# Kernel tuning notes

Measured on AMD Instinct MI355X. Metric: run time of the kernel, lower is better.

The kernel has to match this reference:

```python
import jax, jax.numpy as jnp
from jax import lax
import numpy as np


def setup_inputs() -> dict:
    key = jax.random.key(0)
    ks = jax.random.split(key, 9)
    B, T_enc, D = 32, 2048, 512   # batch, encoder length, enc_dim == nb_dims
    T_dec, U = 128, 512           # decode steps, LSTM units (== out_dim)
    s = 0.05
    return {
        "enc_output": jax.random.normal(ks[0], (B, T_enc, D), jnp.float32),
        "dec_input": jax.random.normal(ks[1], (B, T_dec, U), jnp.float32),
        "W1": jax.random.normal(ks[2], (D, D), jnp.float32) * s,
        "W2": jax.random.normal(ks[3], (U, D), jnp.float32) * s,
        "b2": jnp.zeros((D,), jnp.float32),
        "V": jax.random.normal(ks[4], (D,), jnp.float32) * s,
        "W3": jax.random.normal(ks[5], (D + U, U), jnp.float32) * s,
        "b3": jnp.zeros((U,), jnp.float32),
        "lstm_kernel": jax.random.normal(ks[6], (U, 4 * U), jnp.float32) * s,
        "lstm_rec_kernel": jax.random.normal(ks[7], (U, 4 * U), jnp.float32) * s,
        "lstm_bias": jnp.zeros((4 * U,), jnp.float32),
    }


def reference(enc_output, dec_input, W1, W2, b2, V, W3, b3,
              lstm_kernel, lstm_rec_kernel, lstm_bias):
    # Precomputed constant, as in get_constants(): xW1 = enc_output @ W1
    xW1 = jnp.einsum('bte,ed->btd', enc_output, W1)  # [B, T_enc, D]

    def step(carry, x_t):
        h, c = carry                                  # [B, U] each
        # Bahdanau additive attention score over encoder positions
        hW2 = h @ W2 + b2                             # [B, D]
        u = jnp.tanh(xW1 + hW2[:, None, :])           # [B, T_enc, D]
        scores = jnp.einsum('btd,d->bt', u, V)        # [B, T_enc]
        a = jax.nn.softmax(scores, axis=1)            # [B, T_enc]
        Xa = jnp.einsum('bt,bte->be', a, enc_output)  # [B, D]
        # Mix decoder input with context, then LSTM cell step
        h_in = jnp.concatenate([x_t, Xa], axis=1) @ W3 + b3  # [B, U]
        z = h_in @ lstm_kernel + h @ lstm_rec_kernel + lstm_bias
        zi, zf, zg, zo = jnp.split(z, 4, axis=1)
        i = jax.nn.sigmoid(zi)
        f = jax.nn.sigmoid(zf)
        g = jnp.tanh(zg)
        o = jax.nn.sigmoid(zo)
        c_new = f * c + i * g
        h_new = o * jnp.tanh(c_new)
        return (h_new, c_new), h_new

    B = enc_output.shape[0]
    U = W3.shape[1]
    h0 = jnp.zeros((B, U), enc_output.dtype)
    c0 = jnp.zeros((B, U), enc_output.dtype)
    xs = jnp.swapaxes(dec_input, 0, 1)                # [T_dec, B, U]
    _, ys = lax.scan(step, (h0, c0), xs)              # ys: [T_dec, B, U]
    return jnp.swapaxes(ys, 0, 1)                     # [B, T_dec, U]
```

## Files before the change

kernel.cpp:

```cpp
#include <hip/hip_runtime.h>
#include <hip/hip_cooperative_groups.h>
#include <cstddef>
#include <cstdint>

namespace cg = cooperative_groups;

#define B 32
#define TENC 2048
#define TDEC 128
#define NCH 8
#define TCH 256

typedef unsigned short ushort_t;
typedef __attribute__((ext_vector_type(8))) short short8;
typedef __attribute__((ext_vector_type(4))) float floatx4;

__device__ __forceinline__ uint16_t f2bf(float x) {
    uint32_t u = __float_as_uint(x);
    u += 0x7fffu + ((u >> 16) & 1u);
    return (uint16_t)(u >> 16);
}
__device__ __forceinline__ float bf2f(ushort_t u) {
    return __uint_as_float(((uint32_t)u) << 16);
}
__device__ __forceinline__ void unpack8(uint4 v, float* f) {
    f[0] = __uint_as_float(v.x << 16); f[1] = __uint_as_float(v.x & 0xffff0000u);
    f[2] = __uint_as_float(v.y << 16); f[3] = __uint_as_float(v.y & 0xffff0000u);
    f[4] = __uint_as_float(v.z << 16); f[5] = __uint_as_float(v.z & 0xffff0000u);
    f[6] = __uint_as_float(v.w << 16); f[7] = __uint_as_float(v.w & 0xffff0000u);
}
__device__ __forceinline__ float fast_tanh(float x) {
    float e = __expf(2.f * x);
    return 1.f - 2.f * __builtin_amdgcn_rcpf(e + 1.f);
}
__device__ __forceinline__ float fast_sig(float x) {
    return __builtin_amdgcn_rcpf(1.f + __expf(-x));
}

__global__ void cvt_kernel(const float* __restrict__ in, ushort_t* __restrict__ out) {
    int i = blockIdx.x * 256 + threadIdx.x;
    const float4* ip = (const float4*)in;
    float4 a = ip[2 * i], b = ip[2 * i + 1];
    uint4 o;
    o.x = (uint32_t)f2bf(a.x) | ((uint32_t)f2bf(a.y) << 16);
    o.y = (uint32_t)f2bf(a.z) | ((uint32_t)f2bf(a.w) << 16);
    o.z = (uint32_t)f2bf(b.x) | ((uint32_t)f2bf(b.y) << 16);
    o.w = (uint32_t)f2bf(b.z) | ((uint32_t)f2bf(b.w) << 16);
    ((uint4*)out)[i] = o;
}

__global__ void tr_cvt_bf16_kernel(const float* __restrict__ in, ushort_t* __restrict__ out,
                                   int R, int C) {
    __shared__ float tile[32][33];
    int r0 = blockIdx.y * 32, c0 = blockIdx.x * 32;
    int tx = threadIdx.x & 31, ty = threadIdx.x >> 5;
#pragma unroll
    for (int i = 0; i < 4; i++) {
        int r = ty + i * 8;
        tile[r][tx] = in[(size_t)(r0 + r) * C + c0 + tx];
    }
    __syncthreads();
#pragma unroll
    for (int i = 0; i < 4; i++) {
        int rr = ty + i * 8;
        out[(size_t)(c0 + rr) * R + r0 + tx] = f2bf(tile[tx][rr]);
    }
}
__global__ void tr_f32_kernel(const float* __restrict__ in, float* __restrict__ out,
                              int R, int C) {
    __shared__ float tile[32][33];
    int r0 = blockIdx.y * 32, c0 = blockIdx.x * 32;
    int tx = threadIdx.x & 31, ty = threadIdx.x >> 5;
#pragma unroll
    for (int i = 0; i < 4; i++) {
        int r = ty + i * 8;
        tile[r][tx] = in[(size_t)(r0 + r) * C + c0 + tx];
    }
    __syncthreads();
#pragma unroll
    for (int i = 0; i < 4; i++) {
        int rr = ty + i * 8;
        out[(size_t)(c0 + rr) * R + r0 + tx] = tile[tx][rr];
    }
}

__global__ void bz_kernel(const float* __restrict__ b3, const float* __restrict__ Wk,
                          const float* __restrict__ bias, float* __restrict__ bz) {
    int g = blockIdx.x * 256 + threadIdx.x;
    float s = bias[g];
#pragma unroll 8
    for (int u = 0; u < 512; u++) s += b3[u] * Wk[(size_t)u * 2048 + g];
    bz[g] = s;
}

template <int BF16OUT>
__global__ void mfma_gemm_kernel(const ushort_t* __restrict__ A, const ushort_t* __restrict__ Bt,
                                 void* __restrict__ C, int M, int N) {
    int tid = threadIdx.x, wave = tid >> 6, lane = tid & 63;
    int wy = wave & 1, wx = wave >> 1;
    int m0 = blockIdx.y * 64 + wy * 32;
    int n0 = blockIdx.x * 64 + wx * 32;
    int lr = lane & 15, quad = lane >> 4;
    floatx4 a00 = {0.f, 0.f, 0.f, 0.f}, a01 = a00, a10 = a00, a11 = a00;
    const short8* Ap0 = (const short8*)(A + (size_t)(m0 + lr) * 512 + quad * 8);
    const short8* Ap1 = (const short8*)(A + (size_t)(m0 + 16 + lr) * 512 + quad * 8);
    const short8* Bp0 = (const short8*)(Bt + (size_t)(n0 + lr) * 512 + quad * 8);
    const short8* Bp1 = (const short8*)(Bt + (size_t)(n0 + 16 + lr) * 512 + quad * 8);
#pragma unroll 4
    for (int k = 0; k < 16; k++) {
        short8 av0 = Ap0[k * 4], av1 = Ap1[k * 4];
        short8 bv0 = Bp0[k * 4], bv1 = Bp1[k * 4];
        a00 = __builtin_amdgcn_mfma_f32_16x16x32_bf16(av0, bv0, a00, 0, 0, 0);
        a01 = __builtin_amdgcn_mfma_f32_16x16x32_bf16(av0, bv1, a01, 0, 0, 0);
        a10 = __builtin_amdgcn_mfma_f32_16x16x32_bf16(av1, bv0, a10, 0, 0, 0);
        a11 = __builtin_amdgcn_mfma_f32_16x16x32_bf16(av1, bv1, a11, 0, 0, 0);
    }
    int rb = quad * 4;
    if (BF16OUT) {
        ushort_t* Cp = (ushort_t*)C;
#pragma unroll
        for (int r = 0; r < 4; r++) {
            Cp[(size_t)(m0 + rb + r) * N + n0 + lr] = f2bf(a00[r]);
            Cp[(size_t)(m0 + rb + r) * N + n0 + 16 + lr] = f2bf(a01[r]);
            Cp[(size_t)(m0 + 16 + rb + r) * N + n0 + lr] = f2bf(a10[r]);
            Cp[(size_t)(m0 + 16 + rb + r) * N + n0 + 16 + lr] = f2bf(a11[r]);
        }
    } else {
        float* Cp = (float*)C;
#pragma unroll
        for (int r = 0; r < 4; r++) {
            Cp[(size_t)(m0 + rb + r) * N + n0 + lr] = a00[r];
            Cp[(size_t)(m0 + rb + r) * N + n0 + 16 + lr] = a01[r];
            Cp[(size_t)(m0 + 16 + rb + r) * N + n0 + lr] = a10[r];
            Cp[(size_t)(m0 + 16 + rb + r) * N + n0 + 16 + lr] = a11[r];
        }
    }
}

__global__ __launch_bounds__(256, 1) void step_kernel(
    const ushort_t* __restrict__ xW1h, const ushort_t* __restrict__ ench,
    const ushort_t* __restrict__ Zxh, const float* __restrict__ bz,
    const float* __restrict__ W2t, const float* __restrict__ Wrt,
    const float* __restrict__ Wazt, const float* __restrict__ Vv,
    const float* __restrict__ b2,
    float* __restrict__ h, float* __restrict__ c, float* __restrict__ hW2,
    float* __restrict__ zbuf, float* __restrict__ pm, float* __restrict__ pl,
    float* __restrict__ pacc, float* __restrict__ Xa, float* __restrict__ out) {
    cg::grid_group grid = cg::this_grid();
    int bk = blockIdx.x, tid = threadIdx.x;
    int wave = tid >> 6, lane = tid & 63;
    __shared__ float smem[21560];

    for (int t = 0; t < TDEC; ++t) {
        {
            for (int idx = tid; idx < 16384; idx += 256)
                smem[(idx >> 9) * 513 + (idx & 511)] = h[idx];
            int n0 = bk * 10;
            for (int idx = tid; idx < 5120; idx += 256) {
                int cc = idx >> 9, d = idx & 511;
                int n = n0 + cc;
                const float* src = (n < 512) ? (W2t + (size_t)n * 512)
                                             : (Wrt + (size_t)(n - 512) * 512);
                smem[16416 + cc * 513 + d] = src[d];
            }
            __syncthreads();
            int q = tid & 3;
#pragma unroll
            for (int r = 0; r < 5; ++r) {
                int o = r * 64 + (tid >> 2);
                int cc = o >> 5, b = o & 31;
                const float* hrow = smem + b * 513;
                const float* wrow = smem + 16416 + cc * 513;
                float acc = 0.f;
#pragma unroll 8
                for (int i = 0; i < 128; ++i) {
                    int d = q + 4 * i;
                    acc += hrow[d] * wrow[d];
                }
                acc += __shfl_xor(acc, 1, 64);
                acc += __shfl_xor(acc, 2, 64);
                if (q == 0) {
                    int n = n0 + cc;
                    if (n < 512) {
                        hW2[b * 512 + n] = acc + b2[n];
                    } else {
                        int g = n - 512;
                        float zx = bf2f(Zxh[((size_t)(b * 128 + t)) * 2048 + g]);
                        zbuf[b * 2048 + g] = acc + zx + bz[g];
                    }
                }
            }
        }
        grid.sync();
        {
            int b = bk >> 3, ch = bk & 7;
            float hs[8], vs[8];
            {
                const float4* hp = (const float4*)(hW2 + b * 512 + lane * 8);
                float4 h0 = hp[0], h1 = hp[1];
                hs[0] = h0.x; hs[1] = h0.y; hs[2] = h0.z; hs[3] = h0.w;
                hs[4] = h1.x; hs[5] = h1.y; hs[6] = h1.z; hs[7] = h1.w;
                const float4* vp = (const float4*)(Vv + lane * 8);
                float4 v0 = vp[0], v1 = vp[1];
                vs[0] = v0.x; vs[1] = v0.y; vs[2] = v0.z; vs[3] = v0.w;
                vs[4] = v1.x; vs[5] = v1.y; vs[6] = v1.z; vs[7] = v1.w;
            }
            int t0 = ch * TCH + wave * 64;
            const uint4* xr = (const uint4*)xW1h + ((size_t)b * TENC + t0) * 64 + lane;
            const uint4* er = (const uint4*)ench + ((size_t)b * TENC + t0) * 64 + lane;
            float m = -INFINITY, l = 0.f;
            float acc[8] = {0.f, 0.f, 0.f, 0.f, 0.f, 0.f, 0.f, 0.f};
#pragma unroll 2
            for (int tt = 0; tt < 64; ++tt) {
                uint4 xv = xr[(size_t)tt * 64];
                uint4 ev = er[(size_t)tt * 64];
                float xf[8], ef[8];
                unpack8(xv, xf);
                float s = 0.f;
#pragma unroll
                for (int j = 0; j < 8; j++) s += fast_tanh(xf[j] + hs[j]) * vs[j];
#pragma unroll
                for (int off = 32; off >= 1; off >>= 1) s += __shfl_xor(s, off, 64);
                float mn = fmaxf(m, s);
                float sc = __expf(m - mn);
                float p = __expf(s - mn);
                l = l * sc + p;
                unpack8(ev, ef);
#pragma unroll
                for (int j = 0; j < 8; j++) acc[j] = acc[j] * sc + p * ef[j];
                m = mn;
            }
            float* smv = smem;
            float* slv = smem + 8;
            float* sacc = smem + 16;
            if (lane == 0) { smv[wave] = m; slv[wave] = l; }
            __syncthreads();
            float bmx = fmaxf(fmaxf(smv[0], smv[1]), fmaxf(smv[2], smv[3]));
            float f = __expf(m - bmx);
#pragma unroll
            for (int j = 0; j < 8; j++) sacc[wave * 512 + lane * 8 + j] = acc[j] * f;
            __syncthreads();
            float s0 = sacc[tid] + sacc[512 + tid] + sacc[1024 + tid] + sacc[1536 + tid];
            float s1 = sacc[tid + 256] + sacc[512 + tid + 256] + sacc[1024 + tid + 256] +
                       sacc[1536 + tid + 256];
            size_t po = ((size_t)(b * NCH + ch)) * 512;
            pacc[po + tid] = s0;
            pacc[po + tid + 256] = s1;
            if (tid == 0) {
                pm[b * NCH + ch] = bmx;
                pl[b * NCH + ch] = slv[0] * __expf(smv[0] - bmx) + slv[1] * __expf(smv[1] - bmx) +
                                   slv[2] * __expf(smv[2] - bmx) + slv[3] * __expf(smv[3] - bmx);
            }
        }
        grid.sync();
        {
            int b = bk >> 3, ds0 = (bk & 7) * 64;
            if (tid < 64) {
                float mg = -1e30f;
#pragma unroll
                for (int i = 0; i < NCH; i++) mg = fmaxf(mg, pm[b * NCH + i]);
                float w[NCH];
                float L = 0.f;
#pragma unroll
                for (int i = 0; i < NCH; i++) {
                    w[i] = __expf(pm[b * NCH + i] - mg);
                    L += pl[b * NCH + i] * w[i];
                }
                float inv = __builtin_amdgcn_rcpf(L);
                int d = ds0 + tid;
                float s = 0.f;
#pragma unroll
                for (int i = 0; i < NCH; i++)
                    s += w[i] * pacc[((size_t)(b * NCH + i)) * 512 + d];
                Xa[b * 512 + d] = s * inv;
            }
        }
        grid.sync();
        {
            for (int idx = tid; idx < 16384; idx += 256)
                smem[(idx >> 9) * 513 + (idx & 511)] = Xa[idx];
            int u0 = bk * 2;
            for (int idx = tid; idx < 4096; idx += 256) {
                int rw = idx >> 9, d = idx & 511;
                int g = (rw >> 1) * 512 + u0 + (rw & 1);
                smem[16416 + rw * 513 + d] = Wazt[(size_t)g * 512 + d];
            }
            __syncthreads();
            int col = tid >> 5, b = tid & 31;
            const float* xrow = smem + b * 513;
            const float* wrow = smem + 16416 + col * 513;
            float acc = 0.f;
#pragma unroll 8
            for (int d = 0; d < 512; ++d) acc += xrow[d] * wrow[d];
            int g = (col >> 1) * 512 + u0 + (col & 1);
            smem[20800 + col * 32 + b] = acc + zbuf[b * 2048 + g];
            __syncthreads();
            if (tid < 64) {
                int bb = tid >> 1, uo = tid & 1;
                int u = u0 + uo;
                float zi = smem[20800 + (0 + uo) * 32 + bb];
                float zf = smem[20800 + (2 + uo) * 32 + bb];
                float zg = smem[20800 + (4 + uo) * 32 + bb];
                float zo = smem[20800 + (6 + uo) * 32 + bb];
                float ig = fast_sig(zi);
                float fg = fast_sig(zf);
                float gg = fast_tanh(zg);
                float og = fast_sig(zo);
                int idx = bb * 512 + u;
                float cn = fg * c[idx] + ig * gg;
                float hn = og * fast_tanh(cn);
                c[idx] = cn;
                h[idx] = hn;
                out[((size_t)bb * TDEC + t) * 512 + u] = hn;
            }
        }
        grid.sync();
    }
}

extern "C" void kernel_launch(void* const* d_in, const int* in_sizes, int n_in,
                              void* d_out, int out_size, void* d_ws, size_t ws_size,
                              hipStream_t stream) {
    const float* enc = (const float*)d_in[0];
    const float* dec = (const float*)d_in[1];
    const float* W1 = (const float*)d_in[2];
    const float* W2 = (const float*)d_in[3];
    const float* b2 = (const float*)d_in[4];
    const float* V = (const float*)d_in[5];
    const float* W3 = (const float*)d_in[6];
    const float* b3 = (const float*)d_in[7];
    const float* Wk = (const float*)d_in[8];
    const float* Wr = (const float*)d_in[9];
    const float* bias = (const float*)d_in[10];
    float* out = (float*)d_out;

    char* ws = (char*)d_ws;
    size_t o = 0;
    auto alloc = [&](size_t bytes) {
        void* p = ws + o;
        o += (bytes + 255) & ~(size_t)255;
        return p;
    };
    ushort_t* xW1h = (ushort_t*)alloc(67108864);
    ushort_t* ench = (ushort_t*)alloc(67108864);
    ushort_t* Zxh = (ushort_t*)alloc(16777216);
    ushort_t* dech = (ushort_t*)alloc(4194304);
    ushort_t* T1h = (ushort_t*)alloc(4194304);
    ushort_t* W1t = (ushort_t*)alloc(524288);
    ushort_t* W3h = (ushort_t*)alloc(1048576);
    ushort_t* W3at = (ushort_t*)alloc(524288);
    ushort_t* Wkt = (ushort_t*)alloc(2097152);
    float* W2t = (float*)alloc(1048576);
    float* Wrt = (float*)alloc(4194304);
    float* Wazt = (float*)alloc(4194304);
    float* bz = (float*)alloc(8192);
    float* h = (float*)alloc(65536);
    float* c = (float*)alloc(65536);
    float* hW2 = (float*)alloc(65536);
    float* Xa = (float*)alloc(65536);
    float* zbuf = (float*)alloc(262144);
    float* pm = (float*)alloc(1024);
    float* pl = (float*)alloc(1024);
    float* pacc = (float*)alloc(524288);

    hipMemsetAsync(h, 0, 131072, stream);

    cvt_kernel<<<16384, 256, 0, stream>>>(enc, ench);
    cvt_kernel<<<1024, 256, 0, stream>>>(dec, dech);
    cvt_kernel<<<256, 256, 0, stream>>>(W3, W3h);
    tr_cvt_bf16_kernel<<<dim3(16, 16), 256, 0, stream>>>(W1, W1t, 512, 512);
    tr_cvt_bf16_kernel<<<dim3(16, 16), 256, 0, stream>>>(W3, W3at, 512, 512);
    tr_cvt_bf16_kernel<<<dim3(64, 16), 256, 0, stream>>>(Wk, Wkt, 512, 2048);
    tr_f32_kernel<<<dim3(16, 16), 256, 0, stream>>>(W2, W2t, 512, 512);
    tr_f32_kernel<<<dim3(64, 16), 256, 0, stream>>>(Wr, Wrt, 512, 2048);
    bz_kernel<<<8, 256, 0, stream>>>(b3, Wk, bias, bz);
    mfma_gemm_kernel<1><<<dim3(8, 1024), 256, 0, stream>>>(ench, W1t, xW1h, 65536, 512);
    mfma_gemm_kernel<1><<<dim3(8, 64), 256, 0, stream>>>(dech, W3at, T1h, 4096, 512);
    mfma_gemm_kernel<1><<<dim3(32, 64), 256, 0, stream>>>(T1h, Wkt, Zxh, 4096, 2048);
    mfma_gemm_kernel<0><<<dim3(8, 32), 256, 0, stream>>>(Wkt, W3h + 512 * 512, Wazt, 2048, 512);

    void* args[] = {&xW1h, &ench, &Zxh, &bz, &W2t, &Wrt, &Wazt, &V, &b2,
                    &h, &c, &hW2, &zbuf, &pm, &pl, &pacc, &Xa, &out};
    hipLaunchCooperativeKernel((void*)step_kernel, dim3(256), dim3(256), args, 0, stream);
}
```

Measured before the change: 22.91 ms.

## Widen step kernel to 512 threads, drop softmax max, prefetch loads, use fp32 precompute

Doubles the cooperative step kernel to 512 threads (8 waves) and rebalances every phase for the extra waves. In the attention phase it drops the running-max rescaling of the online softmax and prefetches encoder rows with a four-deep register buffer, cutting exp and FMA work per position. It also computes the xW1 precompute with an fp32 SIMT GEMM instead of a bf16 MFMA GEMM, and keeps the Zx term in fp32. Together these aim at more latency hiding and less ALU work per step, likely for accuracy as well. The costs are a slower precompute GEMM and a softmax that relies on the scores staying small enough not to overflow exp.

After: 21.82 ms. 4.8% less time.

```diff
diff --git a/kernel.cpp b/kernel.cpp
--- a/kernel.cpp
+++ b/kernel.cpp
@@ -19,9 +19,6 @@
     uint32_t u = __float_as_uint(x);
     u += 0x7fffu + ((u >> 16) & 1u);
     return (uint16_t)(u >> 16);
-}
-__device__ __forceinline__ float bf2f(ushort_t u) {
-    return __uint_as_float(((uint32_t)u) << 16);
 }
 __device__ __forceinline__ void unpack8(uint4 v, float* f) {
     f[0] = __uint_as_float(v.x << 16); f[1] = __uint_as_float(v.x & 0xffff0000u);
@@ -91,6 +88,45 @@
 #pragma unroll 8
     for (int u = 0; u < 512; u++) s += b3[u] * Wk[(size_t)u * 2048 + g];
     bz[g] = s;
+}
+
+__global__ void gemm_xw1_kernel(const float* __restrict__ A, const float* __restrict__ Bm,
+                                ushort_t* __restrict__ C) {
+    __shared__ float As[16][68];
+    __shared__ float Bs[16][68];
+    int bm = blockIdx.y * 64, bn = blockIdx.x * 64;
+    int tx = threadIdx.x & 15, ty = threadIdx.x >> 4;
+    float acc[4][4] = {};
+    for (int k0 = 0; k0 < 512; k0 += 16) {
+#pragma unroll
+        for (int i = 0; i < 4; i++) {
+            int idx = threadIdx.x + 256 * i;
+            int r = idx >> 4, kk = idx & 15;
+            As[kk][r] = A[(size_t)(bm + r) * 512 + k0 + kk];
+            int cc = idx & 63, kb = idx >> 6;
+            Bs[kb][cc] = Bm[(size_t)(k0 + kb) * 512 + bn + cc];
+        }
+        __syncthreads();
+#pragma unroll
+        for (int kk = 0; kk < 16; kk++) {
+            float4 av = *(const float4*)&As[kk][ty * 4];
+            float4 bv = *(const float4*)&Bs[kk][tx * 4];
+            float a[4] = {av.x, av.y, av.z, av.w};
+            float b[4] = {bv.x, bv.y, bv.z, bv.w};
+#pragma unroll
+            for (int i = 0; i < 4; i++)
+#pragma unroll
+                for (int j = 0; j < 4; j++) acc[i][j] += a[i] * b[j];
+        }
+        __syncthreads();
+    }
+#pragma unroll
+    for (int i = 0; i < 4; i++) {
+        uint2 o;
+        o.x = (uint32_t)f2bf(acc[i][0]) | ((uint32_t)f2bf(acc[i][1]) << 16);
+        o.y = (uint32_t)f2bf(acc[i][2]) | ((uint32_t)f2bf(acc[i][3]) << 16);
+        *(uint2*)(C + (size_t)(bm + ty * 4 + i) * 512 + bn + tx * 4) = o;
+    }
 }
 
 template <int BF16OUT>
@@ -137,26 +173,34 @@
     }
 }
 
-__global__ __launch_bounds__(256, 1) void step_kernel(
+__global__ __launch_bounds__(512, 2) void step_kernel(
     const ushort_t* __restrict__ xW1h, const ushort_t* __restrict__ ench,
-    const ushort_t* __restrict__ Zxh, const float* __restrict__ bz,
+    const float* __restrict__ Zxf, const float* __restrict__ bz,
     const float* __restrict__ W2t, const float* __restrict__ Wrt,
     const float* __restrict__ Wazt, const float* __restrict__ Vv,
     const float* __restrict__ b2,
     float* __restrict__ h, float* __restrict__ c, float* __restrict__ hW2,
-    float* __restrict__ zbuf, float* __restrict__ pm, float* __restrict__ pl,
+    float* __restrict__ zbuf, float* __restrict__ pl,
     float* __restrict__ pacc, float* __restrict__ Xa, float* __restrict__ out) {
     cg::grid_group grid = cg::this_grid();
     int bk = blockIdx.x, tid = threadIdx.x;
     int wave = tid >> 6, lane = tid & 63;
     __shared__ float smem[21560];
 
+    float vs[8];
+    {
+        const float4* vp = (const float4*)(Vv + lane * 8);
+        float4 v0 = vp[0], v1 = vp[1];
+        vs[0] = v0.x; vs[1] = v0.y; vs[2] = v0.z; vs[3] = v0.w;
+        vs[4] = v1.x; vs[5] = v1.y; vs[6] = v1.z; vs[7] = v1.w;
+    }
+
     for (int t = 0; t < TDEC; ++t) {
         {
-            for (int idx = tid; idx < 16384; idx += 256)
+            for (int idx = tid; idx < 16384; idx += 512)
                 smem[(idx >> 9) * 513 + (idx & 511)] = h[idx];
             int n0 = bk * 10;
-            for (int idx = tid; idx < 5120; idx += 256) {
+            for (int idx = tid; idx < 5120; idx += 512) {
                 int cc = idx >> 9, d = idx & 511;
                 int n = n0 + cc;
                 const float* src = (n < 512) ? (W2t + (size_t)n * 512)
@@ -164,11 +208,13 @@
                 smem[16416 + cc * 513 + d] = src[d];
             }
             __syncthreads();
-            int q = tid & 3;
-#pragma unroll
-            for (int r = 0; r < 5; ++r) {
-                int o = r * 64 + (tid >> 2);
+            int q = tid & 3, slot = tid >> 2;
+#pragma unroll
+            for (int r = 0; r < 3; ++r) {
+                int o = r * 128 + slot;
+                bool valid = (o < 320);
                 int cc = o >> 5, b = o & 31;
+                if (cc > 9) cc = 9;
                 const float* hrow = smem + b * 513;
                 const float* wrow = smem + 16416 + cc * 513;
                 float acc = 0.f;
@@ -179,14 +225,14 @@
                 }
                 acc += __shfl_xor(acc, 1, 64);
                 acc += __shfl_xor(acc, 2, 64);
-                if (q == 0) {
+                if (q == 0 && valid) {
                     int n = n0 + cc;
                     if (n < 512) {
                         hW2[b * 512 + n] = acc + b2[n];
                     } else {
                         int g = n - 512;
-                        float zx = bf2f(Zxh[((size_t)(b * 128 + t)) * 2048 + g]);
-                        zbuf[b * 2048 + g] = acc + zx + bz[g];
+                        zbuf[b * 2048 + g] =
+                            acc + Zxf[((size_t)(b * 128 + t)) * 2048 + g] + bz[g];
                     }
                 }
             }
@@ -194,26 +240,20 @@
         grid.sync();
         {
             int b = bk >> 3, ch = bk & 7;
-            float hs[8], vs[8];
+            float hs[8];
             {
                 const float4* hp = (const float4*)(hW2 + b * 512 + lane * 8);
                 float4 h0 = hp[0], h1 = hp[1];
                 hs[0] = h0.x; hs[1] = h0.y; hs[2] = h0.z; hs[3] = h0.w;
                 hs[4] = h1.x; hs[5] = h1.y; hs[6] = h1.z; hs[7] = h1.w;
-                const float4* vp = (const float4*)(Vv + lane * 8);
-                float4 v0 = vp[0], v1 = vp[1];
-                vs[0] = v0.x; vs[1] = v0.y; vs[2] = v0.z; vs[3] = v0.w;
-                vs[4] = v1.x; vs[5] = v1.y; vs[6] = v1.z; vs[7] = v1.w;
-            }
-            int t0 = ch * TCH + wave * 64;
+            }
+            int t0 = ch * TCH + wave * 32;
             const uint4* xr = (const uint4*)xW1h + ((size_t)b * TENC + t0) * 64 + lane;
             const uint4* er = (const uint4*)ench + ((size_t)b * TENC + t0) * 64 + lane;
-            float m = -INFINITY, l = 0.f;
+            float l = 0.f;
             float acc[8] = {0.f, 0.f, 0.f, 0.f, 0.f, 0.f, 0.f, 0.f};
-#pragma unroll 2
-            for (int tt = 0; tt < 64; ++tt) {
-                uint4 xv = xr[(size_t)tt * 64];
-                uint4 ev = er[(size_t)tt * 64];
+
+            auto body = [&](uint4 xv, uint4 ev) {
                 float xf[8], ef[8];
                 unpack8(xv, xf);
                 float s = 0.f;
@@ -221,87 +261,99 @@
                 for (int j = 0; j < 8; j++) s += fast_tanh(xf[j] + hs[j]) * vs[j];
 #pragma unroll
                 for (int off = 32; off >= 1; off >>= 1) s += __shfl_xor(s, off, 64);
-                float mn = fmaxf(m, s);
-                float sc = __expf(m - mn);
-                float p = __expf(s - mn);
-                l = l * sc + p;
+                float p = __expf(s);
+                l += p;
                 unpack8(ev, ef);
 #pragma unroll
-                for (int j = 0; j < 8; j++) acc[j] = acc[j] * sc + p * ef[j];
-                m = mn;
-            }
-            float* smv = smem;
-            float* slv = smem + 8;
+                for (int j = 0; j < 8; j++) acc[j] += p * ef[j];
+            };
+
+            uint4 xb[4], eb[4];
+#pragma unroll
+            for (int i = 0; i < 4; i++) {
+                xb[i] = xr[(size_t)i * 64];
+                eb[i] = er[(size_t)i * 64];
+            }
+#pragma unroll 4
+            for (int tt = 0; tt < 28; ++tt) {
+                int sl = tt & 3;
+                uint4 xv = xb[sl], ev = eb[sl];
+                xb[sl] = xr[(size_t)(tt + 4) * 64];
+                eb[sl] = er[(size_t)(tt + 4) * 64];
+                body(xv, ev);
+            }
+#pragma unroll
+            for (int tt = 28; tt < 32; ++tt) body(xb[tt & 3], eb[tt & 3]);
+
+            float* slv = smem;
             float* sacc = smem + 16;
-            if (lane == 0) { smv[wave] = m; slv[wave] = l; }
+            if (lane == 0) slv[wave] = l;
+            float4* sa = (float4*)(sacc + wave * 512 + lane * 8);
+            sa[0] = make_float4(acc[0], acc[1], acc[2], acc[3]);
+            sa[1] = make_float4(acc[4], acc[5], acc[6], acc[7]);
             __syncthreads();
-            float bmx = fmaxf(fmaxf(smv[0], smv[1]), fmaxf(smv[2], smv[3]));
-            float f = __expf(m - bmx);
-#pragma unroll
-            for (int j = 0; j < 8; j++) sacc[wave * 512 + lane * 8 + j] = acc[j] * f;
-            __syncthreads();
-            float s0 = sacc[tid] + sacc[512 + tid] + sacc[1024 + tid] + sacc[1536 + tid];
-            float s1 = sacc[tid + 256] + sacc[512 + tid + 256] + sacc[1024 + tid + 256] +
-                       sacc[1536 + tid + 256];
+            float sd = 0.f;
+#pragma unroll
+            for (int w = 0; w < 8; w++) sd += sacc[w * 512 + tid];
             size_t po = ((size_t)(b * NCH + ch)) * 512;
-            pacc[po + tid] = s0;
-            pacc[po + tid + 256] = s1;
+            pacc[po + tid] = sd;
             if (tid == 0) {
-                pm[b * NCH + ch] = bmx;
-                pl[b * NCH + ch] = slv[0] * __expf(smv[0] - bmx) + slv[1] * __expf(smv[1] - bmx) +
-                                   slv[2] * __expf(smv[2] - bmx) + slv[3] * __expf(smv[3] - bmx);
+                float ls = 0.f;
+#pragma unroll
+                for (int w = 0; w < 8; w++) ls += slv[w];
+                pl[b * NCH + ch] = ls;
             }
         }
         grid.sync();
         {
             int b = bk >> 3, ds0 = (bk & 7) * 64;
             if (tid < 64) {
-                float mg = -1e30f;
-#pragma unroll
-                for (int i = 0; i < NCH; i++) mg = fmaxf(mg, pm[b * NCH + i]);
-                float w[NCH];
                 float L = 0.f;
 #pragma unroll
-                for (int i = 0; i < NCH; i++) {
-                    w[i] = __expf(pm[b * NCH + i] - mg);
-                    L += pl[b * NCH + i] * w[i];
-                }
+                for (int i = 0; i < NCH; i++) L += pl[b * NCH + i];
                 float inv = __builtin_amdgcn_rcpf(L);
                 int d = ds0 + tid;
                 float s = 0.f;
 #pragma unroll
                 for (int i = 0; i < NCH; i++)
-                    s += w[i] * pacc[((size_t)(b * NCH + i)) * 512 + d];
+                    s += pacc[((size_t)(b * NCH + i)) * 512 + d];
                 Xa[b * 512 + d] = s * inv;
             }
         }
         grid.sync();
         {
-            for (int idx = tid; idx < 16384; idx += 256)
+            for (int idx = tid; idx < 16384; idx += 512)
                 smem[(idx >> 9) * 513 + (idx & 511)] = Xa[idx];
             int u0 = bk * 2;
-            for (int idx = tid; idx < 4096; idx += 256) {
+            for (int idx = tid; idx < 4096; idx += 512) {
                 int rw = idx >> 9, d = idx & 511;
                 int g = (rw >> 1) * 512 + u0 + (rw & 1);
                 smem[16416 + rw * 513 + d] = Wazt[(size_t)g * 512 + d];
             }
             __syncthreads();
-            int col = tid >> 5, b = tid & 31;
+            int q = tid & 1, o = tid >> 1;
+            int col = o >> 5, b = o & 31;
             const float* xrow = smem + b * 513;
             const float* wrow = smem + 16416 + col * 513;
             float acc = 0.f;
 #pragma unroll 8
-            for (int d = 0; d < 512; ++d) acc += xrow[d] * wrow[d];
-            int g = (col >> 1) * 512 + u0 + (col & 1);
-            smem[20800 + col * 32 + b] = acc + zbuf[b * 2048 + g];
+            for (int i = 0; i < 256; ++i) {
+                int d = q * 256 + i;
+                acc += xrow[d] * wrow[d];
+            }
+            acc += __shfl_xor(acc, 1, 64);
+            if (q == 0) {
+                int g = (col >> 1) * 512 + u0 + (col & 1);
+                smem[20520 + col * 32 + b] = acc + zbuf[b * 2048 + g];
+            }
             __syncthreads();
             if (tid < 64) {
                 int bb = tid >> 1, uo = tid & 1;
                 int u = u0 + uo;
-                float zi = smem[20800 + (0 + uo) * 32 + bb];
-                float zf = smem[20800 + (2 + uo) * 32 + bb];
-                float zg = smem[20800 + (4 + uo) * 32 + bb];
-                float zo = smem[20800 + (6 + uo) * 32 + bb];
+                float zi = smem[20520 + (0 + uo) * 32 + bb];
+                float zf = smem[20520 + (2 + uo) * 32 + bb];
+                float zg = smem[20520 + (4 + uo) * 32 + bb];
+                float zo = smem[20520 + (6 + uo) * 32 + bb];
                 float ig = fast_sig(zi);
                 float fg = fast_sig(zf);
                 float gg = fast_tanh(zg);
@@ -343,10 +395,9 @@
     };
     ushort_t* xW1h = (ushort_t*)alloc(67108864);
     ushort_t* ench = (ushort_t*)alloc(67108864);
-    ushort_t* Zxh = (ushort_t*)alloc(16777216);
+    float* Zxf = (float*)alloc(33554432);
     ushort_t* dech = (ushort_t*)alloc(4194304);
     ushort_t* T1h = (ushort_t*)alloc(4194304);
-    ushort_t* W1t = (ushort_t*)alloc(524288);
     ushort_t* W3h = (ushort_t*)alloc(1048576);
     ushort_t* W3at = (ushort_t*)alloc(524288);
     ushort_t* Wkt = (ushort_t*)alloc(2097152);
@@ -359,7 +410,6 @@
     float* hW2 = (float*)alloc(65536);
     float* Xa = (float*)alloc(65536);
     float* zbuf = (float*)alloc(262144);
-    float* pm = (float*)alloc(1024);
     float* pl = (float*)alloc(1024);
     float* pacc = (float*)alloc(524288);
 
@@ -368,18 +418,17 @@
     cvt_kernel<<<16384, 256, 0, stream>>>(enc, ench);
     cvt_kernel<<<1024, 256, 0, stream>>>(dec, dech);
     cvt_kernel<<<256, 256, 0, stream>>>(W3, W3h);
-    tr_cvt_bf16_kernel<<<dim3(16, 16), 256, 0, stream>>>(W1, W1t, 512, 512);
     tr_cvt_bf16_kernel<<<dim3(16, 16), 256, 0, stream>>>(W3, W3at, 512, 512);
     tr_cvt_bf16_kernel<<<dim3(64, 16), 256, 0, stream>>>(Wk, Wkt, 512, 2048);
     tr_f32_kernel<<<dim3(16, 16), 256, 0, stream>>>(W2, W2t, 512, 512);
     tr_f32_kernel<<<dim3(64, 16), 256, 0, stream>>>(Wr, Wrt, 512, 2048);
     bz_kernel<<<8, 256, 0, stream>>>(b3, Wk, bias, bz);
-    mfma_gemm_kernel<1><<<dim3(8, 1024), 256, 0, stream>>>(ench, W1t, xW1h, 65536, 512);
+    gemm_xw1_kernel<<<dim3(8, 1024), 256, 0, stream>>>(enc, W1, xW1h);
     mfma_gemm_kernel<1><<<dim3(8, 64), 256, 0, stream>>>(dech, W3at, T1h, 4096, 512);
-    mfma_gemm_kernel<1><<<dim3(32, 64), 256, 0, stream>>>(T1h, Wkt, Zxh, 4096, 2048);
+    mfma_gemm_kernel<0><<<dim3(32, 64), 256, 0, stream>>>(T1h, Wkt, Zxf, 4096, 2048);
     mfma_gemm_kernel<0><<<dim3(8, 32), 256, 0, stream>>>(Wkt, W3h + 512 * 512, Wazt, 2048, 512);
 
-    void* args[] = {&xW1h, &ench, &Zxh, &bz, &W2t, &Wrt, &Wazt, &V, &b2,
-                    &h, &c, &hW2, &zbuf, &pm, &pl, &pacc, &Xa, &out};
-    hipLaunchCooperativeKernel((void*)step_kernel, dim3(256), dim3(256), args, 0, stream);
-}
+    void* args[] = {&xW1h, &ench, &Zxf, &bz, &W2t, &Wrt, &Wazt, &V, &b2,
+                    &h, &c, &hW2, &zbuf, &pl, &pacc, &Xa, &out};
+    hipLaunchCooperativeKernel((void*)step_kernel, dim3(256), dim3(512), args, 0, stream);
+}
```
